# Kernel tuning notes

Measured on AMD Instinct MI355X. Metric: run time of the kernel, lower is better.

The kernel has to match this reference:

```python
import jax, jax.numpy as jnp
import numpy as np

B, F, P, H1, H2 = 4096, 1024, 64, 256, 128

def setup_inputs() -> dict:
    key = jax.random.key(0)
    ks = jax.random.split(key, 7)
    def glorot(k, shape, fan_in):
        bound = 1.0 / np.sqrt(fan_in)
        return jax.random.uniform(k, shape, jnp.float32, -bound, bound)
    return {
        "features": jax.random.normal(ks[0], (B, F), jnp.float32),
        "W1": glorot(ks[1], (P, F, H1), F),   # stacked per-predicate first-layer weights
        "b1": glorot(ks[2], (P, H1), F),
        "W2": glorot(ks[3], (P, H1, H2), H1),
        "b2": glorot(ks[4], (P, H2), H1),
        "W3": glorot(ks[5], (P, H2), H2),     # last layer out_dim=1, squeezed
        "b3": glorot(ks[6], (P,), H2),
    }

def reference(features, W1, b1, W2, b2, W3, b3):
    # All n_predicates MLPs as batched GEMMs (dropout = identity at inference).
    h1 = jax.nn.relu(jnp.einsum('bf,pfh->pbh', features, W1) + b1[:, None, :])  # [P,B,H1]
    h2 = jax.nn.relu(jnp.einsum('pbh,phk->pbk', h1, W2) + b2[:, None, :])       # [P,B,H2]
    logits = jnp.einsum('pbk,pk->pb', h2, W3) + b3[:, None]                      # [P,B]
    return jax.nn.sigmoid(logits).T  # [B, P] matching torch.cat(dim=1)
```

## Files before the change

### kernel.cpp

```cpp
#include <hip/hip_runtime.h>
#include <hip/hip_bf16.h>

#define B_SZ 4096
#define F_SZ 1024
#define P_SZ 64
#define H1D  256
#define H2D  128

typedef __attribute__((ext_vector_type(8))) short  short8;
typedef __attribute__((ext_vector_type(4))) float  floatx4;
typedef __attribute__((ext_vector_type(2))) float  float2v;
typedef __attribute__((ext_vector_type(4))) float  float4v;

typedef __attribute__((address_space(1))) const void* gas_t;
typedef __attribute__((address_space(3))) void*       las_t;

__device__ __forceinline__ short bfbits(float f) {
  __bf16 h = (__bf16)f;
  return __builtin_bit_cast(short, h);
}

__device__ __forceinline__ void gll16(const void* g, void* l) {
  __builtin_amdgcn_global_load_lds((gas_t)g, (las_t)l, 16, 0, 0);
}

#define WS_A_OFF   0
#define WS_W1_OFF  8388608UL
#define WS_W2_OFF  41943040UL
#define WS_NEEDED  46137344UL

__global__ __launch_bounds__(256) void prep_A(const float* __restrict__ feat,
                                              short8* __restrict__ outv) {
  const int c = blockIdx.x * 256 + threadIdx.x;
  const int row = c & 15, kg = (c >> 4) & 3, f = (c >> 6) & 7, kt = (c >> 9) & 31, mt = c >> 14;
  const float* src = feat + (size_t)(mt * 128 + f * 16 + row) * F_SZ + kt * 32 + kg * 8;
  float4v v0 = *(const float4v*)src;
  float4v v1 = *(const float4v*)(src + 4);
  short8 o;
  #pragma unroll
  for (int j = 0; j < 4; ++j) { o[j] = bfbits(v0[j]); o[4 + j] = bfbits(v1[j]); }
  outv[c] = o;
}

__global__ __launch_bounds__(256) void prep_W1(const float* __restrict__ W1,
                                               short8* __restrict__ outv) {
  const int c = blockIdx.x * 256 + threadIdx.x;
  const int nr = c & 15, kg = (c >> 4) & 3, nf = (c >> 6) & 15, kt = (c >> 10) & 31, p = c >> 15;
  const float* src = W1 + ((size_t)p * F_SZ + kt * 32 + kg * 8) * H1D + nf * 16 + nr;
  short8 o;
  #pragma unroll
  for (int j = 0; j < 8; ++j) o[j] = bfbits(src[(size_t)j * H1D]);
  outv[c] = o;
}

__global__ __launch_bounds__(256) void prep_W2(const float* __restrict__ W2,
                                               short8* __restrict__ outv) {
  const int c = blockIdx.x * 256 + threadIdx.x;
  const int qr = c & 15, kgl = (c >> 4) & 3, ks = (c >> 6) & 1, qf = (c >> 7) & 7,
            kc = (c >> 10) & 3, p = c >> 12;
  const float* src = W2 + ((size_t)p * H1D + kc * 64 + ks * 32 + kgl * 8) * H2D + qf * 16 + qr;
  short8 o;
  #pragma unroll
  for (int j = 0; j < 8; ++j) o[j] = bfbits(src[(size_t)j * H2D]);
  outv[c] = o;
}

__global__ __launch_bounds__(512, 2)
void fused_mlp_v3(const char* __restrict__ ws,
                  const float* __restrict__ b1,
                  const float* __restrict__ b2,
                  const float* __restrict__ W3,
                  const float* __restrict__ b3,
                  float* __restrict__ out) {
  __shared__ __align__(16) char sm[73728];

  const int tid  = threadIdx.x;
  const int lane = tid & 63;
  const int wid  = tid >> 6;
  const int wm   = wid >> 2;
  const int wn   = wid & 3;

  const int bid = blockIdx.x;
  const int wg  = (bid & 7) * 256 + (bid >> 3);
  const int p   = wg >> 5;
  const int mt  = wg & 31;
  const int m0  = mt * 128;

  const char* Apre  = ws + WS_A_OFF  + (size_t)mt * 32 * 512 * 16;
  const char* W1pre = ws + WS_W1_OFF + (size_t)p  * 32 * 1024 * 16;
  const char* W2pre = ws + WS_W2_OFF + (size_t)p  *  4 * 1024 * 16;
  const float* b1p  = b1 + p * H1D;
  const float* b2p  = b2 + p * H2D;
  const float* W3p  = W3 + p * H2D;

  float b1v[4];
  #pragma unroll
  for (int ni = 0; ni < 4; ++ni)
    b1v[ni] = b1p[wn * 64 + ni * 16 + (lane & 15)];

  floatx4 acc[4][4];
  #pragma unroll
  for (int i = 0; i < 4; ++i)
    #pragma unroll
    for (int j = 0; j < 4; ++j)
      acc[i][j] = (floatx4)0.0f;

  auto stage = [&](int ib, int kt) {
    const char* ga = Apre + (size_t)kt * 8192 + tid * 16;
    gll16(ga, sm + ib * 8192 + wid * 1024);
    const char* gb = W1pre + (size_t)kt * 16384 + tid * 16;
    gll16(gb,        sm + 24576 + ib * 16384 + wid * 1024);
    gll16(gb + 8192, sm + 24576 + ib * 16384 + 8192 + wid * 1024);
  };

  stage(0, 0);
  stage(1, 1);
  asm volatile("s_waitcnt vmcnt(3)" ::: "memory");
  __builtin_amdgcn_s_barrier();

  int ibr = 0;
  for (int t = 0; t < 32; ++t) {
    short8 af[4], bfr[4];
    #pragma unroll
    for (int mi = 0; mi < 4; ++mi)
      af[mi] = *(const short8*)(sm + ibr * 8192 + ((wm * 4 + mi) * 64 + lane) * 16);
    #pragma unroll
    for (int ni = 0; ni < 4; ++ni)
      bfr[ni] = *(const short8*)(sm + 24576 + ibr * 16384 + ((wn * 4 + ni) * 64 + lane) * 16);

    const int ibs = (ibr == 0) ? 2 : ibr - 1;
    if (t + 2 < 32) stage(ibs, t + 2);

    __builtin_amdgcn_s_setprio(1);
    #pragma unroll
    for (int mi = 0; mi < 4; ++mi)
      #pragma unroll
      for (int ni = 0; ni < 4; ++ni)
        acc[mi][ni] = __builtin_amdgcn_mfma_f32_16x16x32_bf16(af[mi], bfr[ni], acc[mi][ni], 0, 0, 0);
    __builtin_amdgcn_s_setprio(0);

    if (t + 1 < 32) {
      if (t + 2 < 32) {
        asm volatile("s_waitcnt vmcnt(3)" ::: "memory");
      } else {
        asm volatile("s_waitcnt vmcnt(0)" ::: "memory");
      }
      __builtin_amdgcn_s_barrier();
    }
    ibr = (ibr == 2) ? 0 : ibr + 1;
  }
  __syncthreads();

  floatx4 acc2[4][2];
  #pragma unroll
  for (int mi = 0; mi < 4; ++mi)
    #pragma unroll
    for (int qi = 0; qi < 2; ++qi)
      acc2[mi][qi] = (floatx4)0.0f;

  for (int kc = 0; kc < 4; ++kc) {
    const char* gw = W2pre + (size_t)kc * 16384 + tid * 16;
    gll16(gw,        sm + 16384 + wid * 1024);
    gll16(gw + 8192, sm + 16384 + 8192 + wid * 1024);
    if (wn == kc) {
      #pragma unroll
      for (int mi = 0; mi < 4; ++mi) {
        #pragma unroll
        for (int ni = 0; ni < 4; ++ni) {
          const int kl = ni * 16 + (lane & 15);
          const int base = (((wm * 4 + mi) * 2 + (kl >> 5)) * 64 + ((kl >> 3) & 3) * 16) * 16
                           + (kl & 7) * 2;
          #pragma unroll
          for (int r = 0; r < 4; ++r) {
            float v = fmaxf(acc[mi][ni][r] + b1v[ni], 0.0f);
            const int row = (lane >> 4) * 4 + r;
            *(short*)(sm + base + row * 16) = bfbits(v);
          }
        }
      }
    }
    __syncthreads();
    #pragma unroll
    for (int ks = 0; ks < 2; ++ks) {
      short8 hf[4], wf[2];
      #pragma unroll
      for (int mi = 0; mi < 4; ++mi)
        hf[mi] = *(const short8*)(sm + (((wm * 4 + mi) * 2 + ks) * 64 + lane) * 16);
      #pragma unroll
      for (int qi = 0; qi < 2; ++qi)
        wf[qi] = *(const short8*)(sm + 16384 + (((wn * 2 + qi) * 2 + ks) * 64 + lane) * 16);
      #pragma unroll
      for (int mi = 0; mi < 4; ++mi)
        #pragma unroll
        for (int qi = 0; qi < 2; ++qi)
          acc2[mi][qi] = __builtin_amdgcn_mfma_f32_16x16x32_bf16(hf[mi], wf[qi], acc2[mi][qi], 0, 0, 0);
    }
    __syncthreads();
  }

  float lsum[4][4];
  #pragma unroll
  for (int mi = 0; mi < 4; ++mi)
    #pragma unroll
    for (int r = 0; r < 4; ++r) lsum[mi][r] = 0.0f;

  #pragma unroll
  for (int qi = 0; qi < 2; ++qi) {
    const int q = wn * 32 + qi * 16 + (lane & 15);
    const float b2v = b2p[q];
    const float w3v = W3p[q];
    #pragma unroll
    for (int mi = 0; mi < 4; ++mi)
      #pragma unroll
      for (int r = 0; r < 4; ++r) {
        const float h = fmaxf(acc2[mi][qi][r] + b2v, 0.0f);
        lsum[mi][r] += h * w3v;
      }
  }
  #pragma unroll
  for (int mask = 1; mask <= 8; mask <<= 1)
    #pragma unroll
    for (int mi = 0; mi < 4; ++mi)
      #pragma unroll
      for (int r = 0; r < 4; ++r)
        lsum[mi][r] += __shfl_xor(lsum[mi][r], mask, 64);

  float* part = (float*)(sm + 32768);
  if ((lane & 15) == 0) {
    const int g = lane >> 4;
    #pragma unroll
    for (int mi = 0; mi < 4; ++mi)
      #pragma unroll
      for (int r = 0; r < 4; ++r)
        part[wn * 128 + wm * 64 + mi * 16 + g * 4 + r] = lsum[mi][r];
  }
  __syncthreads();
  if (tid < 128) {
    const float x = part[tid] + part[128 + tid] + part[256 + tid] + part[384 + tid] + b3[p];
    const float s = 1.0f / (1.0f + __expf(-x));
    out[(size_t)(m0 + tid) * P_SZ + p] = s;
  }
}

__global__ __launch_bounds__(512, 2)
void fused_mlp_kernel(const float* __restrict__ feat,
                      const float* __restrict__ W1,
                      const float* __restrict__ b1,
                      const float* __restrict__ W2,
                      const float* __restrict__ b2,
                      const float* __restrict__ W3,
                      const float* __restrict__ b3,
                      float* __restrict__ out) {
  __shared__ __align__(16) char sm[49152];
  const int tid  = threadIdx.x;
  const int lane = tid & 63;
  const int wid  = tid >> 6;
  const int wm   = wid >> 2;
  const int wn   = wid & 3;
  const int bid = blockIdx.x;
  const int wg  = (bid & 7) * 256 + (bid >> 3);
  const int p   = wg >> 5;
  const int mt  = wg & 31;
  const int m0  = mt * 128;

  const float* featm = feat + (size_t)m0 * F_SZ;
  const float* W1p   = W1 + (size_t)p * F_SZ * H1D;
  const float* b1p   = b1 + p * H1D;
  const float* W2p   = W2 + (size_t)p * H1D * H2D;
  const float* b2p   = b2 + p * H2D;
  const float* W3p   = W3 + p * H2D;

  const int a_m  = tid >> 2;
  const int a_kg = tid & 3;
  const int b_n2 = tid & 127;
  const int b_kq = tid >> 7;

  float a_reg[8];
  float b_reg[16];
  floatx4 acc[4][4];
  #pragma unroll
  for (int i = 0; i < 4; ++i)
    #pragma unroll
    for (int j = 0; j < 4; ++j)
      acc[i][j] = (floatx4)0.0f;

  auto stage_load = [&](int k0) {
    const float* pa = featm + a_m * F_SZ + k0 + a_kg * 8;
    *(float4v*)(&a_reg[0]) = *(const float4v*)(pa);
    *(float4v*)(&a_reg[4]) = *(const float4v*)(pa + 4);
    #pragma unroll
    for (int i = 0; i < 8; ++i) {
      const float* pb = W1p + (size_t)(k0 + b_kq * 8 + i) * H1D + b_n2 * 2;
      *(float2v*)(&b_reg[2 * i]) = *(const float2v*)(pb);
    }
  };
  auto stage_write = [&](int cur) {
    short8 av;
    #pragma unroll
    for (int i = 0; i < 8; ++i) av[i] = bfbits(a_reg[i]);
    const int aslot = (a_m >> 4) * 64 + (a_m & 15) + a_kg * 16;
    *(short8*)(sm + cur * 8192 + aslot * 16) = av;
    #pragma unroll
    for (int dn = 0; dn < 2; ++dn) {
      short8 bv;
      #pragma unroll
      for (int i = 0; i < 8; ++i) bv[i] = bfbits(b_reg[2 * i + dn]);
      const int n = b_n2 * 2 + dn;
      const int bslot = (n >> 4) * 64 + (n & 15) + b_kq * 16;
      *(short8*)(sm + 16384 + cur * 16384 + bslot * 16) = bv;
    }
  };
  auto compute = [&](int cur) {
    short8 af[4], bfr[4];
    #pragma unroll
    for (int mi = 0; mi < 4; ++mi)
      af[mi] = *(const short8*)(sm + cur * 8192 + ((wm * 4 + mi) * 64 + lane) * 16);
    #pragma unroll
    for (int ni = 0; ni < 4; ++ni)
      bfr[ni] = *(const short8*)(sm + 16384 + cur * 16384 + ((wn * 4 + ni) * 64 + lane) * 16);
    #pragma unroll
    for (int mi = 0; mi < 4; ++mi)
      #pragma unroll
      for (int ni = 0; ni < 4; ++ni)
        acc[mi][ni] = __builtin_amdgcn_mfma_f32_16x16x32_bf16(af[mi], bfr[ni], acc[mi][ni], 0, 0, 0);
  };

  stage_load(0);
  stage_write(0);
  __syncthreads();
  int cur = 0;
  for (int t = 0; t < 32; ++t) {
    if (t + 1 < 32) stage_load((t + 1) * 32);
    compute(cur);
    if (t + 1 < 32) stage_write(cur ^ 1);
    __syncthreads();
    cur ^= 1;
  }

  floatx4 acc2[4][2];
  #pragma unroll
  for (int mi = 0; mi < 4; ++mi)
    #pragma unroll
    for (int qi = 0; qi < 2; ++qi)
      acc2[mi][qi] = (floatx4)0.0f;

  float b1v[4];
  #pragma unroll
  for (int ni = 0; ni < 4; ++ni)
    b1v[ni] = b1p[wn * 64 + ni * 16 + (lane & 15)];

  const int w2_q2 = tid & 63;
  const int w2_kq = tid >> 6;

  for (int kc = 0; kc < 4; ++kc) {
    const int kbase = kc * 64;
    float w2reg[16];
    #pragma unroll
    for (int i = 0; i < 8; ++i) {
      const float* pw = W2p + (size_t)(kbase + w2_kq * 8 + i) * H2D + w2_q2 * 2;
      *(float2v*)(&w2reg[2 * i]) = *(const float2v*)(pw);
    }
    #pragma unroll
    for (int dq = 0; dq < 2; ++dq) {
      short8 wv;
      #pragma unroll
      for (int i = 0; i < 8; ++i) wv[i] = bfbits(w2reg[2 * i + dq]);
      const int q = w2_q2 * 2 + dq;
      const int slot = ((q >> 4) * 2 + (w2_kq >> 2)) * 64 + (w2_kq & 3) * 16 + (q & 15);
      *(short8*)(sm + 16384 + slot * 16) = wv;
    }
    if (wn == kc) {
      #pragma unroll
      for (int mi = 0; mi < 4; ++mi) {
        #pragma unroll
        for (int ni = 0; ni < 4; ++ni) {
          const int kl = ni * 16 + (lane & 15);
          const int base = (((wm * 4 + mi) * 2 + (kl >> 5)) * 64 + ((kl >> 3) & 3) * 16) * 16
                           + (kl & 7) * 2;
          #pragma unroll
          for (int r = 0; r < 4; ++r) {
            float v = fmaxf(acc[mi][ni][r] + b1v[ni], 0.0f);
            const int row = (lane >> 4) * 4 + r;
            *(short*)(sm + base + row * 16) = bfbits(v);
          }
        }
      }
    }
    __syncthreads();
    #pragma unroll
    for (int ks = 0; ks < 2; ++ks) {
      short8 hf[4], wf[2];
      #pragma unroll
      for (int mi = 0; mi < 4; ++mi)
        hf[mi] = *(const short8*)(sm + (((wm * 4 + mi) * 2 + ks) * 64 + lane) * 16);
      #pragma unroll
      for (int qi = 0; qi < 2; ++qi)
        wf[qi] = *(const short8*)(sm + 16384 + (((wn * 2 + qi) * 2 + ks) * 64 + lane) * 16);
      #pragma unroll
      for (int mi = 0; mi < 4; ++mi)
        #pragma unroll
        for (int qi = 0; qi < 2; ++qi)
          acc2[mi][qi] = __builtin_amdgcn_mfma_f32_16x16x32_bf16(hf[mi], wf[qi], acc2[mi][qi], 0, 0, 0);
    }
    __syncthreads();
  }

  float lsum[4][4];
  #pragma unroll
  for (int mi = 0; mi < 4; ++mi)
    #pragma unroll
    for (int r = 0; r < 4; ++r) lsum[mi][r] = 0.0f;

  #pragma unroll
  for (int qi = 0; qi < 2; ++qi) {
    const int q = wn * 32 + qi * 16 + (lane & 15);
    const float b2v = b2p[q];
    const float w3v = W3p[q];
    #pragma unroll
    for (int mi = 0; mi < 4; ++mi)
      #pragma unroll
      for (int r = 0; r < 4; ++r) {
        const float h = fmaxf(acc2[mi][qi][r] + b2v, 0.0f);
        lsum[mi][r] += h * w3v;
      }
  }
  #pragma unroll
  for (int mask = 1; mask <= 8; mask <<= 1)
    #pragma unroll
    for (int mi = 0; mi < 4; ++mi)
      #pragma unroll
      for (int r = 0; r < 4; ++r)
        lsum[mi][r] += __shfl_xor(lsum[mi][r], mask, 64);

  float* part = (float*)(sm + 32768);
  if ((lane & 15) == 0) {
    const int g = lane >> 4;
    #pragma unroll
    for (int mi = 0; mi < 4; ++mi)
      #pragma unroll
      for (int r = 0; r < 4; ++r)
        part[wn * 128 + wm * 64 + mi * 16 + g * 4 + r] = lsum[mi][r];
  }
  __syncthreads();
  if (tid < 128) {
    const float x = part[tid] + part[128 + tid] + part[256 + tid] + part[384 + tid] + b3[p];
    const float s = 1.0f / (1.0f + __expf(-x));
    out[(size_t)(m0 + tid) * P_SZ + p] = s;
  }
}

extern "C" void kernel_launch(void* const* d_in, const int* in_sizes, int n_in,
                              void* d_out, int out_size, void* d_ws, size_t ws_size,
                              hipStream_t stream) {
  (void)in_sizes; (void)n_in; (void)out_size;
  const float* feat = (const float*)d_in[0];
  const float* W1   = (const float*)d_in[1];
  const float* b1   = (const float*)d_in[2];
  const float* W2   = (const float*)d_in[3];
  const float* b2   = (const float*)d_in[4];
  const float* W3   = (const float*)d_in[5];
  const float* b3   = (const float*)d_in[6];
  float* out = (float*)d_out;

  if (ws_size >= WS_NEEDED) {
    char* ws = (char*)d_ws;
    hipLaunchKernelGGL(prep_A,  dim3(2048), dim3(256), 0, stream, feat, (short8*)(ws + WS_A_OFF));
    hipLaunchKernelGGL(prep_W1, dim3(8192), dim3(256), 0, stream, W1,   (short8*)(ws + WS_W1_OFF));
    hipLaunchKernelGGL(prep_W2, dim3(1024), dim3(256), 0, stream, W2,   (short8*)(ws + WS_W2_OFF));
    hipLaunchKernelGGL(fused_mlp_v3, dim3(2048), dim3(512), 0, stream,
                       (const char*)ws, b1, b2, W3, b3, out);
  } else {
    hipLaunchKernelGGL(fused_mlp_kernel, dim3(2048), dim3(512), 0, stream,
                       feat, W1, b1, W2, b2, W3, b3, out);
  }
}
```

Baseline: 187.7 us.

## Double M tile to 256 rows and prefetch all W2 during layer-1 tail

The fused MLP kernel now processes 256 batch rows per workgroup instead of 128, halving the grid and doubling reuse of each W1/W2 tile loaded per predicate. The entire W2 slice is prefetched into LDS during the last two layer-1 iterations, replacing the per-chunk W2 loads and barriers in layer 2. Layer 2 is restructured into two halves that write all H1 activations to LDS at once. LDS grows to about 132 KB and accumulator registers double, which likely limits occupancy to one workgroup per CU despite the launch bounds.

```diff
diff --git a/kernel.cpp b/kernel.cpp
--- a/kernel.cpp
+++ b/kernel.cpp
@@ -66,13 +66,13 @@
 }
 
 __global__ __launch_bounds__(512, 2)
-void fused_mlp_v3(const char* __restrict__ ws,
+void fused_mlp_v5(const char* __restrict__ ws,
                   const float* __restrict__ b1,
                   const float* __restrict__ b2,
                   const float* __restrict__ W3,
                   const float* __restrict__ b3,
                   float* __restrict__ out) {
-  __shared__ __align__(16) char sm[73728];
+  __shared__ __align__(16) char sm[135168];
 
   const int tid  = threadIdx.x;
   const int lane = tid & 63;
@@ -81,116 +81,117 @@
   const int wn   = wid & 3;
 
   const int bid = blockIdx.x;
-  const int wg  = (bid & 7) * 256 + (bid >> 3);
-  const int p   = wg >> 5;
-  const int mt  = wg & 31;
-  const int m0  = mt * 128;
-
-  const char* Apre  = ws + WS_A_OFF  + (size_t)mt * 32 * 512 * 16;
-  const char* W1pre = ws + WS_W1_OFF + (size_t)p  * 32 * 1024 * 16;
-  const char* W2pre = ws + WS_W2_OFF + (size_t)p  *  4 * 1024 * 16;
-  const float* b1p  = b1 + p * H1D;
-  const float* b2p  = b2 + p * H2D;
-  const float* W3p  = W3 + p * H2D;
-
-  float b1v[4];
-  #pragma unroll
-  for (int ni = 0; ni < 4; ++ni)
-    b1v[ni] = b1p[wn * 64 + ni * 16 + (lane & 15)];
-
-  floatx4 acc[4][4];
-  #pragma unroll
-  for (int i = 0; i < 4; ++i)
+  const int wg  = (bid & 7) * 128 + (bid >> 3);
+  const int p   = wg >> 4;
+  const int mt  = wg & 15;
+  const int m0  = mt * 256;
+
+  const char* Apre  = ws + WS_A_OFF  + (size_t)(2 * mt) * 262144;
+  const char* W1pre = ws + WS_W1_OFF + (size_t)p * 524288;
+  const char* W2pre = ws + WS_W2_OFF + (size_t)p * 65536;
+
+  floatx4 acc[8][4];
+  #pragma unroll
+  for (int i = 0; i < 8; ++i)
     #pragma unroll
     for (int j = 0; j < 4; ++j)
       acc[i][j] = (floatx4)0.0f;
 
   auto stage = [&](int ib, int kt) {
-    const char* ga = Apre + (size_t)kt * 8192 + tid * 16;
-    gll16(ga, sm + ib * 8192 + wid * 1024);
+    char* base = sm + ib * 32768;
+    gll16(Apre + (size_t)kt * 8192 + tid * 16,          base + wid * 1024);
+    gll16(Apre + 262144 + (size_t)kt * 8192 + tid * 16, base + 8192 + wid * 1024);
     const char* gb = W1pre + (size_t)kt * 16384 + tid * 16;
-    gll16(gb,        sm + 24576 + ib * 16384 + wid * 1024);
-    gll16(gb + 8192, sm + 24576 + ib * 16384 + 8192 + wid * 1024);
+    gll16(gb,        base + 16384 + wid * 1024);
+    gll16(gb + 8192, base + 24576 + wid * 1024);
   };
 
   stage(0, 0);
   stage(1, 1);
-  asm volatile("s_waitcnt vmcnt(3)" ::: "memory");
+  asm volatile("s_waitcnt vmcnt(4)" ::: "memory");
   __builtin_amdgcn_s_barrier();
 
   int ibr = 0;
   for (int t = 0; t < 32; ++t) {
-    short8 af[4], bfr[4];
-    #pragma unroll
-    for (int mi = 0; mi < 4; ++mi)
-      af[mi] = *(const short8*)(sm + ibr * 8192 + ((wm * 4 + mi) * 64 + lane) * 16);
+    short8 af[8], bfr[4];
+    #pragma unroll
+    for (int mi = 0; mi < 8; ++mi)
+      af[mi] = *(const short8*)(sm + ibr * 32768 + (wm * 8 + mi) * 1024 + lane * 16);
     #pragma unroll
     for (int ni = 0; ni < 4; ++ni)
-      bfr[ni] = *(const short8*)(sm + 24576 + ibr * 16384 + ((wn * 4 + ni) * 64 + lane) * 16);
+      bfr[ni] = *(const short8*)(sm + ibr * 32768 + 16384 + (wn * 4 + ni) * 1024 + lane * 16);
 
     const int ibs = (ibr == 0) ? 2 : ibr - 1;
-    if (t + 2 < 32) stage(ibs, t + 2);
+    if (t < 30) {
+      stage(ibs, t + 2);
+    } else {
+      const int j0 = (t - 30) * 4;
+      #pragma unroll
+      for (int j = 0; j < 4; ++j)
+        gll16(W2pre + (size_t)(j0 + j) * 8192 + tid * 16,
+              sm + 65536 + (j0 + j) * 8192 + wid * 1024);
+    }
 
     __builtin_amdgcn_s_setprio(1);
     #pragma unroll
-    for (int mi = 0; mi < 4; ++mi)
+    for (int mi = 0; mi < 8; ++mi)
       #pragma unroll
       for (int ni = 0; ni < 4; ++ni)
         acc[mi][ni] = __builtin_amdgcn_mfma_f32_16x16x32_bf16(af[mi], bfr[ni], acc[mi][ni], 0, 0, 0);
     __builtin_amdgcn_s_setprio(0);
 
-    if (t + 1 < 32) {
-      if (t + 2 < 32) {
-        asm volatile("s_waitcnt vmcnt(3)" ::: "memory");
-      } else {
-        asm volatile("s_waitcnt vmcnt(0)" ::: "memory");
-      }
+    if (t < 31) {
+      asm volatile("s_waitcnt vmcnt(4)" ::: "memory");
       __builtin_amdgcn_s_barrier();
     }
     ibr = (ibr == 2) ? 0 : ibr + 1;
   }
   __syncthreads();
 
-  floatx4 acc2[4][2];
-  #pragma unroll
-  for (int mi = 0; mi < 4; ++mi)
+  float b1v[4];
+  #pragma unroll
+  for (int ni = 0; ni < 4; ++ni)
+    b1v[ni] = b1[p * H1D + wn * 64 + ni * 16 + (lane & 15)];
+
+  floatx4 acc2[8][2];
+  #pragma unroll
+  for (int mi = 0; mi < 8; ++mi)
     #pragma unroll
     for (int qi = 0; qi < 2; ++qi)
       acc2[mi][qi] = (floatx4)0.0f;
 
-  for (int kc = 0; kc < 4; ++kc) {
-    const char* gw = W2pre + (size_t)kc * 16384 + tid * 16;
-    gll16(gw,        sm + 16384 + wid * 1024);
-    gll16(gw + 8192, sm + 16384 + 8192 + wid * 1024);
-    if (wn == kc) {
-      #pragma unroll
-      for (int mi = 0; mi < 4; ++mi) {
+  const int c  = lane & 15;
+  const int hi = lane >> 4;
+
+  #pragma unroll
+  for (int h = 0; h < 2; ++h) {
+    #pragma unroll
+    for (int mi = 0; mi < 8; ++mi)
+      #pragma unroll
+      for (int ii = 0; ii < 2; ++ii) {
+        const int ni  = h * 2 + ii;
+        const int kg2 = ii * 2 + (c >> 3);
+        const int base = (wn * 16 + wm * 8 + mi) * 1024 + kg2 * 256 + (c & 7) * 2;
         #pragma unroll
-        for (int ni = 0; ni < 4; ++ni) {
-          const int kl = ni * 16 + (lane & 15);
-          const int base = (((wm * 4 + mi) * 2 + (kl >> 5)) * 64 + ((kl >> 3) & 3) * 16) * 16
-                           + (kl & 7) * 2;
-          #pragma unroll
-          for (int r = 0; r < 4; ++r) {
-            float v = fmaxf(acc[mi][ni][r] + b1v[ni], 0.0f);
-            const int row = (lane >> 4) * 4 + r;
-            *(short*)(sm + base + row * 16) = bfbits(v);
-          }
+        for (int r = 0; r < 4; ++r) {
+          const float v = fmaxf(acc[mi][ni][r] + b1v[ni], 0.0f);
+          *(short*)(sm + base + (hi * 4 + r) * 16) = bfbits(v);
         }
       }
-    }
     __syncthreads();
-    #pragma unroll
-    for (int ks = 0; ks < 2; ++ks) {
-      short8 hf[4], wf[2];
-      #pragma unroll
-      for (int mi = 0; mi < 4; ++mi)
-        hf[mi] = *(const short8*)(sm + (((wm * 4 + mi) * 2 + ks) * 64 + lane) * 16);
+
+    #pragma unroll
+    for (int s = 0; s < 4; ++s) {
+      short8 hf[8], wf[2];
+      #pragma unroll
+      for (int mi = 0; mi < 8; ++mi)
+        hf[mi] = *(const short8*)(sm + (s * 16 + wm * 8 + mi) * 1024 + lane * 16);
       #pragma unroll
       for (int qi = 0; qi < 2; ++qi)
-        wf[qi] = *(const short8*)(sm + 16384 + (((wn * 2 + qi) * 2 + ks) * 64 + lane) * 16);
-      #pragma unroll
-      for (int mi = 0; mi < 4; ++mi)
+        wf[qi] = *(const short8*)(sm + 65536 + s * 16384 + (wn * 2 + qi) * 2048
+                                  + h * 1024 + lane * 16);
+      #pragma unroll
+      for (int mi = 0; mi < 8; ++mi)
         #pragma unroll
         for (int qi = 0; qi < 2; ++qi)
           acc2[mi][qi] = __builtin_amdgcn_mfma_f32_16x16x32_bf16(hf[mi], wf[qi], acc2[mi][qi], 0, 0, 0);
@@ -198,45 +199,44 @@
     __syncthreads();
   }
 
-  float lsum[4][4];
-  #pragma unroll
-  for (int mi = 0; mi < 4; ++mi)
+  float lsum[8][4];
+  #pragma unroll
+  for (int mi = 0; mi < 8; ++mi)
     #pragma unroll
     for (int r = 0; r < 4; ++r) lsum[mi][r] = 0.0f;
 
   #pragma unroll
   for (int qi = 0; qi < 2; ++qi) {
-    const int q = wn * 32 + qi * 16 + (lane & 15);
-    const float b2v = b2p[q];
-    const float w3v = W3p[q];
-    #pragma unroll
-    for (int mi = 0; mi < 4; ++mi)
+    const int q = wn * 32 + qi * 16 + c;
+    const float b2v = b2[p * H2D + q];
+    const float w3v = W3[p * H2D + q];
+    #pragma unroll
+    for (int mi = 0; mi < 8; ++mi)
       #pragma unroll
       for (int r = 0; r < 4; ++r) {
-        const float h = fmaxf(acc2[mi][qi][r] + b2v, 0.0f);
-        lsum[mi][r] += h * w3v;
+        const float h2v = fmaxf(acc2[mi][qi][r] + b2v, 0.0f);
+        lsum[mi][r] += h2v * w3v;
       }
   }
   #pragma unroll
   for (int mask = 1; mask <= 8; mask <<= 1)
     #pragma unroll
-    for (int mi = 0; mi < 4; ++mi)
+    for (int mi = 0; mi < 8; ++mi)
       #pragma unroll
       for (int r = 0; r < 4; ++r)
         lsum[mi][r] += __shfl_xor(lsum[mi][r], mask, 64);
 
-  float* part = (float*)(sm + 32768);
-  if ((lane & 15) == 0) {
-    const int g = lane >> 4;
-    #pragma unroll
-    for (int mi = 0; mi < 4; ++mi)
+  float* part = (float*)(sm + 131072);
+  if (c == 0) {
+    #pragma unroll
+    for (int mi = 0; mi < 8; ++mi)
       #pragma unroll
       for (int r = 0; r < 4; ++r)
-        part[wn * 128 + wm * 64 + mi * 16 + g * 4 + r] = lsum[mi][r];
+        part[wn * 256 + wm * 128 + mi * 16 + hi * 4 + r] = lsum[mi][r];
   }
   __syncthreads();
-  if (tid < 128) {
-    const float x = part[tid] + part[128 + tid] + part[256 + tid] + part[384 + tid] + b3[p];
+  if (tid < 256) {
+    const float x = part[tid] + part[256 + tid] + part[512 + tid] + part[768 + tid] + b3[p];
     const float s = 1.0f / (1.0f + __expf(-x));
     out[(size_t)(m0 + tid) * P_SZ + p] = s;
   }
@@ -467,7 +467,7 @@
     hipLaunchKernelGGL(prep_A,  dim3(2048), dim3(256), 0, stream, feat, (short8*)(ws + WS_A_OFF));
     hipLaunchKernelGGL(prep_W1, dim3(8192), dim3(256), 0, stream, W1,   (short8*)(ws + WS_W1_OFF));
     hipLaunchKernelGGL(prep_W2, dim3(1024), dim3(256), 0, stream, W2,   (short8*)(ws + WS_W2_OFF));
-    hipLaunchKernelGGL(fused_mlp_v3, dim3(2048), dim3(512), 0, stream,
+    hipLaunchKernelGGL(fused_mlp_v5, dim3(1024), dim3(512), 0, stream,
                        (const char*)ws, b1, b2, W3, b3, out);
   } else {
     hipLaunchKernelGGL(fused_mlp_kernel, dim3(2048), dim3(512), 0, stream,
```

Measured after the change: 162.0 us. -13.7%, faster.
